# Performance work log

Measured on AMD Instinct MI355X. Metric: run time of the kernel, lower is better.

The kernel has to match this reference:

```python
import jax, jax.numpy as jnp
import numpy as np

L = 2          # num_hidden_layers
B, S, H = 2, 2048, 1024
NH, DH = 16, 64   # heads, head dim
FF = 4096
EPS = 1e-5


def setup_inputs() -> dict:
    key = jax.random.key(0)
    ks = jax.random.split(key, 20)
    s = 0.02
    inp = {
        "hidden_states": jax.random.normal(ks[0], (B, S, H), jnp.float32),
        "attention_mask": jnp.zeros((B, 1, 1, S), jnp.float32),
        "Wq": jax.random.normal(ks[1], (L, H, H), jnp.float32) * s,
        "bq": jnp.zeros((L, H), jnp.float32),
        "Wk": jax.random.normal(ks[2], (L, H, H), jnp.float32) * s,
        "bk": jnp.zeros((L, H), jnp.float32),
        "Wv": jax.random.normal(ks[3], (L, H, H), jnp.float32) * s,
        "bv": jnp.zeros((L, H), jnp.float32),
        "Wao": jax.random.normal(ks[4], (L, H, H), jnp.float32) * s,
        "bao": jnp.zeros((L, H), jnp.float32),
        "ln1_g": jnp.ones((L, H), jnp.float32),
        "ln1_b": jnp.zeros((L, H), jnp.float32),
        "Wi": jax.random.normal(ks[5], (L, H, FF), jnp.float32) * s,
        "bi": jnp.zeros((L, FF), jnp.float32),
        "Wo": jax.random.normal(ks[6], (L, FF, H), jnp.float32) * s,
        "bo": jnp.zeros((L, H), jnp.float32),
        "ln2_g": jnp.ones((L, H), jnp.float32),
        "ln2_b": jnp.zeros((L, H), jnp.float32),
    }
    return inp


def _layernorm(x, g, b):
    m = jnp.mean(x, axis=-1, keepdims=True)
    v = jnp.var(x, axis=-1, keepdims=True)
    return (x - m) * jax.lax.rsqrt(v + EPS) * g + b


def _split_heads(x):
    # [B,S,H] -> [B,NH,S,DH]
    return x.reshape(B, S, NH, DH).transpose(0, 2, 1, 3)


def _layer(x, mask, Wq, bq, Wk, bk, Wv, bv, Wao, bao, g1, b1, Wi, bi, Wo, bo, g2, b2):
    q = _split_heads(x @ Wq + bq)
    k = _split_heads(x @ Wk + bk)
    v = _split_heads(x @ Wv + bv)
    scores = jnp.einsum('bhqd,bhkd->bhqk', q, k) / np.sqrt(DH).astype(np.float32)
    scores = scores + mask  # additive attention mask
    probs = jax.nn.softmax(scores, axis=-1)
    ctx = jnp.einsum('bhqk,bhkd->bhqd', probs, v)
    ctx = ctx.transpose(0, 2, 1, 3).reshape(B, S, H)
    x = _layernorm(ctx @ Wao + bao + x, g1, b1)
    ffn = jax.nn.gelu(x @ Wi + bi, approximate=False) @ Wo + bo
    return _layernorm(ffn + x, g2, b2)


def reference(hidden_states, attention_mask, Wq, bq, Wk, bk, Wv, bv, Wao, bao,
              ln1_g, ln1_b, Wi, bi, Wo, bo, ln2_g, ln2_b):
    x = hidden_states
    for i in range(L):
        x = _layer(x, attention_mask,
                   Wq[i], bq[i], Wk[i], bk[i], Wv[i], bv[i], Wao[i], bao[i],
                   ln1_g[i], ln1_b[i], Wi[i], bi[i], Wo[i], bo[i], ln2_g[i], ln2_b[i])
    return x
```

## Files before the change

### kernel.cpp

```cpp
#include <hip/hip_runtime.h>

typedef _Float16 half_t;
typedef _Float16 half8  __attribute__((ext_vector_type(8)));
typedef _Float16 half4v __attribute__((ext_vector_type(4)));
typedef float    f32x4  __attribute__((ext_vector_type(4)));

#define AS1 __attribute__((address_space(1)))
#define AS3 __attribute__((address_space(3)))

#define MODE_H16  0
#define MODE_F32R 1
#define MODE_GELU 2

__device__ __forceinline__ f32x4 zero4() {
    f32x4 z; z[0] = 0.f; z[1] = 0.f; z[2] = 0.f; z[3] = 0.f; return z;
}

__device__ __forceinline__ half8 lds_frag(const half_t* p) {
    union { uint4 u; half8 h; } c;
    c.u = *(const uint4*)p;
    return c.h;
}

__device__ __forceinline__ void gl_lds16(const half_t* g, half_t* l) {
    __builtin_amdgcn_global_load_lds(
        (AS1 unsigned int*)(unsigned long long)(const void*)g,
        (AS3 unsigned int*)l,
        16, 0, 0);
}

__global__ __launch_bounds__(256) void gemm_bt(
    const half_t* __restrict__ A,
    const half_t* __restrict__ Bt,
    const float*  __restrict__ bias,
    const float*  __restrict__ res,
    void* __restrict__ out,
    int M, int N, int K, int mode)
{
    __shared__ __align__(16) half_t As[128 * 32];
    __shared__ __align__(16) half_t Bs[128 * 32];

    const int tid  = threadIdx.x;
    const int w    = tid >> 6, lane = tid & 63;
    const int m0   = blockIdx.y * 128, n0 = blockIdx.x * 128;
    const int lr   = lane >> 2;
    const int lc   = (lane & 3) * 8;
    const int g    = lane >> 4, ml = lane & 15;
    const int mo   = (w >> 1) * 64, no = (w & 1) * 64;

    f32x4 acc[4][4];
#pragma unroll
    for (int i = 0; i < 4; i++)
#pragma unroll
        for (int j = 0; j < 4; j++) acc[i][j] = zero4();

    const half_t* Ag = A  + (size_t)m0 * K;
    const half_t* Bg = Bt + (size_t)n0 * K;

    for (int k0 = 0; k0 < K; k0 += 32) {
        __syncthreads();
#pragma unroll
        for (int i = 0; i < 2; i++) {
            int r = (w * 2 + i) * 16 + lr;
            gl_lds16(Ag + (size_t)r * K + k0 + lc, &As[(w * 2 + i) * 512]);
            gl_lds16(Bg + (size_t)r * K + k0 + lc, &Bs[(w * 2 + i) * 512]);
        }
        __syncthreads();

        half8 af[4], bf[4];
#pragma unroll
        for (int i = 0; i < 4; i++) af[i] = lds_frag(&As[(mo + i * 16 + ml) * 32 + g * 8]);
#pragma unroll
        for (int j = 0; j < 4; j++) bf[j] = lds_frag(&Bs[(no + j * 16 + ml) * 32 + g * 8]);
#pragma unroll
        for (int i = 0; i < 4; i++)
#pragma unroll
            for (int j = 0; j < 4; j++)
                acc[i][j] = __builtin_amdgcn_mfma_f32_16x16x32_f16(af[i], bf[j], acc[i][j], 0, 0, 0);
    }

    const int gm0 = m0 + mo, gn0 = n0 + no;
#pragma unroll
    for (int j = 0; j < 4; j++) {
        int col = gn0 + j * 16 + ml;
        float bv = bias[col];
#pragma unroll
        for (int i = 0; i < 4; i++) {
#pragma unroll
            for (int r = 0; r < 4; r++) {
                int row = gm0 + i * 16 + g * 4 + r;
                float v = acc[i][j][r] + bv;
                size_t idx = (size_t)row * N + col;
                if (mode == MODE_F32R) {
                    ((float*)out)[idx] = v + res[idx];
                } else if (mode == MODE_GELU) {
                    v = 0.5f * v * (1.f + erff(v * 0.70710678118654752f));
                    ((half_t*)out)[idx] = (half_t)v;
                } else {
                    ((half_t*)out)[idx] = (half_t)v;
                }
            }
        }
    }
}

__global__ __launch_bounds__(256) void gemm_bt64(
    const half_t* __restrict__ A,
    const half_t* __restrict__ Bt,
    const float*  __restrict__ bias,
    const float*  __restrict__ res,
    float* __restrict__ out,
    int M, int N, int K)
{
    __shared__ __align__(16) half_t As[128 * 32];
    __shared__ __align__(16) half_t Bs[64 * 32];

    const int tid  = threadIdx.x;
    const int w    = tid >> 6, lane = tid & 63;
    const int m0   = blockIdx.y * 128, n0 = blockIdx.x * 64;
    const int lr   = lane >> 2, lc = (lane & 3) * 8;
    const int g    = lane >> 4, ml = lane & 15;
    const int mo   = w * 32;

    f32x4 acc[2][4];
#pragma unroll
    for (int i = 0; i < 2; i++)
#pragma unroll
        for (int j = 0; j < 4; j++) acc[i][j] = zero4();

    const half_t* Ag = A  + (size_t)m0 * K;
    const half_t* Bg = Bt + (size_t)n0 * K;

    for (int k0 = 0; k0 < K; k0 += 32) {
        __syncthreads();
#pragma unroll
        for (int i = 0; i < 2; i++)
            gl_lds16(Ag + (size_t)((w * 2 + i) * 16 + lr) * K + k0 + lc, &As[(w * 2 + i) * 512]);
        gl_lds16(Bg + (size_t)(w * 16 + lr) * K + k0 + lc, &Bs[w * 512]);
        __syncthreads();

        half8 af[2], bf[4];
#pragma unroll
        for (int i = 0; i < 2; i++) af[i] = lds_frag(&As[(mo + i * 16 + ml) * 32 + g * 8]);
#pragma unroll
        for (int j = 0; j < 4; j++) bf[j] = lds_frag(&Bs[(j * 16 + ml) * 32 + g * 8]);
#pragma unroll
        for (int i = 0; i < 2; i++)
#pragma unroll
            for (int j = 0; j < 4; j++)
                acc[i][j] = __builtin_amdgcn_mfma_f32_16x16x32_f16(af[i], bf[j], acc[i][j], 0, 0, 0);
    }

    const int gm0 = m0 + mo;
#pragma unroll
    for (int j = 0; j < 4; j++) {
        int col = n0 + j * 16 + ml;
        float bv = bias[col];
#pragma unroll
        for (int i = 0; i < 2; i++) {
#pragma unroll
            for (int r = 0; r < 4; r++) {
                int row = gm0 + i * 16 + g * 4 + r;
                size_t idx = (size_t)row * N + col;
                out[idx] = acc[i][j][r] + bv + res[idx];
            }
        }
    }
}

__global__ __launch_bounds__(256) void gemm_qkv(
    const half_t* __restrict__ A,
    const half_t* __restrict__ Bt,
    const float*  __restrict__ bq,
    const float*  __restrict__ bk,
    const float*  __restrict__ bv,
    half_t* __restrict__ Qo, half_t* __restrict__ Ko, half_t* __restrict__ Vto,
    int M, int K)
{
    __shared__ __align__(16) half_t As[128 * 32];
    __shared__ __align__(16) half_t Bs[128 * 32];

    const int tid  = threadIdx.x;
    const int w    = tid >> 6, lane = tid & 63;
    const int m0   = blockIdx.y * 128, n0 = blockIdx.x * 128;
    const int lr   = lane >> 2, lc = (lane & 3) * 8;
    const int g    = lane >> 4, ml = lane & 15;
    const int mo   = (w >> 1) * 64, no = (w & 1) * 64;

    f32x4 acc[4][4];
#pragma unroll
    for (int i = 0; i < 4; i++)
#pragma unroll
        for (int j = 0; j < 4; j++) acc[i][j] = zero4();

    const half_t* Ag = A  + (size_t)m0 * K;
    const half_t* Bg = Bt + (size_t)n0 * K;

    for (int k0 = 0; k0 < K; k0 += 32) {
        __syncthreads();
#pragma unroll
        for (int i = 0; i < 2; i++) {
            int r = (w * 2 + i) * 16 + lr;
            gl_lds16(Ag + (size_t)r * K + k0 + lc, &As[(w * 2 + i) * 512]);
            gl_lds16(Bg + (size_t)r * K + k0 + lc, &Bs[(w * 2 + i) * 512]);
        }
        __syncthreads();

        half8 af[4], bf[4];
#pragma unroll
        for (int i = 0; i < 4; i++) af[i] = lds_frag(&As[(mo + i * 16 + ml) * 32 + g * 8]);
#pragma unroll
        for (int j = 0; j < 4; j++) bf[j] = lds_frag(&Bs[(no + j * 16 + ml) * 32 + g * 8]);
#pragma unroll
        for (int i = 0; i < 4; i++)
#pragma unroll
            for (int j = 0; j < 4; j++)
                acc[i][j] = __builtin_amdgcn_mfma_f32_16x16x32_f16(af[i], bf[j], acc[i][j], 0, 0, 0);
    }

    const int seg  = n0 >> 10;
    const int nloc = (n0 & 1023) + no;
    const float* bias = (seg == 0) ? bq : (seg == 1) ? bk : bv;
    const int gm0 = m0 + mo;

    if (seg < 2) {
        half_t* O = (seg == 0) ? Qo : Ko;
#pragma unroll
        for (int j = 0; j < 4; j++) {
            int col = nloc + j * 16 + ml;
            float bvv = bias[col];
#pragma unroll
            for (int i = 0; i < 4; i++)
#pragma unroll
                for (int r = 0; r < 4; r++)
                    O[(size_t)(gm0 + i * 16 + g * 4 + r) * 1024 + col] =
                        (half_t)(acc[i][j][r] + bvv);
        }
    } else {
#pragma unroll
        for (int j = 0; j < 4; j++) {
            int col = nloc + j * 16 + ml;
            float bvv = bias[col];
#pragma unroll
            for (int i = 0; i < 4; i++) {
                int rowb = gm0 + i * 16 + g * 4;
                int bb = rowb >> 11, sl = rowb & 2047;
                half4v v;
#pragma unroll
                for (int r = 0; r < 4; r++) v[r] = (half_t)(acc[i][j][r] + bvv);
                *(half4v*)&Vto[((size_t)bb * 1024 + col) * 2048 + sl] = v;
            }
        }
    }
}

__global__ __launch_bounds__(256, 2) void flash_attn(
    const half_t* __restrict__ Q,
    const half_t* __restrict__ Kq,
    const half_t* __restrict__ Vt,
    const float*  __restrict__ mask,
    half_t* __restrict__ ctx,
    int S, int H)
{
    __shared__ __align__(16) half_t Ks[64 * 64];
    __shared__ __align__(16) half_t Vs[64 * 64];
    __shared__ __align__(16) half_t Ps[4 * 32 * 64];

    const int qt = blockIdx.x, h = blockIdx.y, b = blockIdx.z;
    const int tid = threadIdx.x, w = tid >> 6, lane = tid & 63;
    const int g = lane >> 4, ml = lane & 15, m7 = ml & 7;

    const int q0 = qt * 128 + w * 32;
    const half_t* Qg = Q  + ((size_t)(b * S + q0)) * H + h * 64;
    const half_t* Kg = Kq + ((size_t)b * S) * H + h * 64;
    const half_t* Vg = Vt + ((size_t)b * H + h * 64) * (size_t)S;
    const float*  mk = mask + (size_t)b * S;

    half8 qf[2][2];
#pragma unroll
    for (int qi = 0; qi < 2; qi++)
#pragma unroll
        for (int kk = 0; kk < 2; kk++)
            qf[qi][kk] = *(const half8*)(Qg + (size_t)(qi * 16 + ml) * H + kk * 32 + g * 8);

    float m_[2] = {-1e30f, -1e30f}, l_[2] = {0.f, 0.f};
    f32x4 o[2][4];
#pragma unroll
    for (int qi = 0; qi < 2; qi++)
#pragma unroll
        for (int df = 0; df < 4; df++) o[qi][df] = zero4();

    half_t* Pw = &Ps[w * 32 * 64];
    const int srow = tid >> 3;
    const int sc   = tid & 7;

    for (int kv0 = 0; kv0 < S; kv0 += 64) {
        __syncthreads();
#pragma unroll
        for (int t = 0; t < 2; t++) {
            int row = t * 32 + srow;
            int ck  = sc ^ (row & 7);
            gl_lds16(Kg + (size_t)(kv0 + row) * H + ck * 8, &Ks[(t * 256 + w * 64) * 8]);
            gl_lds16(Vg + (size_t)row * S + kv0 + ck * 8,   &Vs[(t * 256 + w * 64) * 8]);
        }
        __syncthreads();

        f32x4 s[2][4];
#pragma unroll
        for (int kvf = 0; kvf < 4; kvf++) {
            half8 k0 = lds_frag(&Ks[(kvf * 16 + ml) * 64 + ((0 + g) ^ m7) * 8]);
            half8 k1 = lds_frag(&Ks[(kvf * 16 + ml) * 64 + ((4 + g) ^ m7) * 8]);
            s[0][kvf] = __builtin_amdgcn_mfma_f32_16x16x32_f16(k0, qf[0][0], zero4(), 0, 0, 0);
            s[0][kvf] = __builtin_amdgcn_mfma_f32_16x16x32_f16(k1, qf[0][1], s[0][kvf], 0, 0, 0);
            s[1][kvf] = __builtin_amdgcn_mfma_f32_16x16x32_f16(k0, qf[1][0], zero4(), 0, 0, 0);
            s[1][kvf] = __builtin_amdgcn_mfma_f32_16x16x32_f16(k1, qf[1][1], s[1][kvf], 0, 0, 0);
        }
#pragma unroll
        for (int kvf = 0; kvf < 4; kvf++) {
            float4 mv = *(const float4*)(mk + kv0 + kvf * 16 + g * 4);
#pragma unroll
            for (int qi = 0; qi < 2; qi++) {
                s[qi][kvf][0] = s[qi][kvf][0] * 0.125f + mv.x;
                s[qi][kvf][1] = s[qi][kvf][1] * 0.125f + mv.y;
                s[qi][kvf][2] = s[qi][kvf][2] * 0.125f + mv.z;
                s[qi][kvf][3] = s[qi][kvf][3] * 0.125f + mv.w;
            }
        }
        float alpha[2];
#pragma unroll
        for (int qi = 0; qi < 2; qi++) {
            float mx = -1e30f;
#pragma unroll
            for (int kvf = 0; kvf < 4; kvf++)
#pragma unroll
                for (int r = 0; r < 4; r++) mx = fmaxf(mx, s[qi][kvf][r]);
            mx = fmaxf(mx, __shfl_xor(mx, 16));
            mx = fmaxf(mx, __shfl_xor(mx, 32));
            float mnew = fmaxf(m_[qi], mx);
            alpha[qi]  = __expf(m_[qi] - mnew);
            m_[qi] = mnew;
            float ps = 0.f;
#pragma unroll
            for (int kvf = 0; kvf < 4; kvf++)
#pragma unroll
                for (int r = 0; r < 4; r++) {
                    float pv = __expf(s[qi][kvf][r] - mnew);
                    s[qi][kvf][r] = pv; ps += pv;
                }
            ps += __shfl_xor(ps, 16);
            ps += __shfl_xor(ps, 32);
            l_[qi] = l_[qi] * alpha[qi] + ps;
#pragma unroll
            for (int kvf = 0; kvf < 4; kvf++) {
                half4v pk;
#pragma unroll
                for (int r = 0; r < 4; r++) pk[r] = (half_t)s[qi][kvf][r];
                *(half4v*)(Pw + (qi * 16 + ml) * 64 +
                           (((kvf * 2 + (g >> 1)) ^ m7) * 8) + (g & 1) * 4) = pk;
            }
        }
#pragma unroll
        for (int qi = 0; qi < 2; qi++) {
#pragma unroll
            for (int r = 0; r < 4; r++) {
                float a = __shfl(alpha[qi], (lane & 48) + g * 4 + r);
#pragma unroll
                for (int df = 0; df < 4; df++) o[qi][df][r] *= a;
            }
        }
#pragma unroll
        for (int kk = 0; kk < 2; kk++) {
            half8 pa0 = lds_frag(&Pw[(ml)      * 64 + ((kk * 4 + g) ^ m7) * 8]);
            half8 pa1 = lds_frag(&Pw[(16 + ml) * 64 + ((kk * 4 + g) ^ m7) * 8]);
#pragma unroll
            for (int df = 0; df < 4; df++) {
                half8 vb = lds_frag(&Vs[(df * 16 + ml) * 64 + ((kk * 4 + g) ^ m7) * 8]);
                o[0][df] = __builtin_amdgcn_mfma_f32_16x16x32_f16(pa0, vb, o[0][df], 0, 0, 0);
                o[1][df] = __builtin_amdgcn_mfma_f32_16x16x32_f16(pa1, vb, o[1][df], 0, 0, 0);
            }
        }
    }

#pragma unroll
    for (int qi = 0; qi < 2; qi++) {
        float inv = 1.f / l_[qi];
#pragma unroll
        for (int r = 0; r < 4; r++) {
            float iv = __shfl(inv, (lane & 48) + g * 4 + r);
            int row = b * S + q0 + qi * 16 + g * 4 + r;
#pragma unroll
            for (int df = 0; df < 4; df++)
                ctx[(size_t)row * H + h * 64 + df * 16 + ml] = (half_t)(o[qi][df][r] * iv);
        }
    }
}

__global__ __launch_bounds__(256) void transpose_cast(
    const float* __restrict__ W, half_t* __restrict__ Wt, int Kd, int Nd)
{
    __shared__ float tile[32][33];
    size_t zoff = (size_t)blockIdx.z * Kd * Nd;
    const float* Wz = W + zoff;
    half_t* Wtz = Wt + zoff;
    int n0 = blockIdx.x * 32, k0 = blockIdx.y * 32;
    int tx = threadIdx.x & 31, ty = threadIdx.x >> 5;
#pragma unroll
    for (int j = 0; j < 4; j++)
        tile[ty + j * 8][tx] = Wz[(size_t)(k0 + ty + j * 8) * Nd + n0 + tx];
    __syncthreads();
#pragma unroll
    for (int j = 0; j < 4; j++)
        Wtz[(size_t)(n0 + ty + j * 8) * Kd + k0 + tx] = (half_t)tile[tx][ty + j * 8];
}

__global__ __launch_bounds__(256) void transpose_qkv(
    const float* __restrict__ Wq, const float* __restrict__ Wk,
    const float* __restrict__ Wv, half_t* __restrict__ WT)
{
    __shared__ float tile[32][33];
    int z = blockIdx.z, l = z / 3, which = z % 3;
    const float* W = ((which == 0) ? Wq : (which == 1) ? Wk : Wv) + (size_t)l * 1024 * 1024;
    half_t* D = WT + ((size_t)l * 3 + which) * 1024 * 1024;
    int n0 = blockIdx.x * 32, k0 = blockIdx.y * 32;
    int tx = threadIdx.x & 31, ty = threadIdx.x >> 5;
#pragma unroll
    for (int j = 0; j < 4; j++)
        tile[ty + j * 8][tx] = W[(size_t)(k0 + ty + j * 8) * 1024 + n0 + tx];
    __syncthreads();
#pragma unroll
    for (int j = 0; j < 4; j++)
        D[(size_t)(n0 + ty + j * 8) * 1024 + k0 + tx] = (half_t)tile[tx][ty + j * 8];
}

__global__ __launch_bounds__(256) void cast_f32_f16(
    const float* __restrict__ in, half_t* __restrict__ out)
{
    int i = blockIdx.x * 256 + threadIdx.x;
    float4 v = ((const float4*)in)[i];
    half4v o; o[0] = (half_t)v.x; o[1] = (half_t)v.y; o[2] = (half_t)v.z; o[3] = (half_t)v.w;
    *(half4v*)(out + (size_t)i * 4) = o;
}

__global__ __launch_bounds__(256) void layernorm_k(
    const float* __restrict__ in,
    const float* __restrict__ gam, const float* __restrict__ bet,
    float* __restrict__ outf, half_t* __restrict__ outh)
{
    int row = blockIdx.x, tid = threadIdx.x;
    const float4 v = ((const float4*)(in + (size_t)row * 1024))[tid];
    float s = v.x + v.y + v.z + v.w;
    float q = v.x * v.x + v.y * v.y + v.z * v.z + v.w * v.w;
    for (int off = 32; off; off >>= 1) { s += __shfl_down(s, off); q += __shfl_down(q, off); }
    __shared__ float ss[4], sq[4];
    int w = tid >> 6;
    if ((tid & 63) == 0) { ss[w] = s; sq[w] = q; }
    __syncthreads();
    float S_ = ss[0] + ss[1] + ss[2] + ss[3];
    float Q_ = sq[0] + sq[1] + sq[2] + sq[3];
    float mean = S_ * (1.f / 1024.f);
    float var  = Q_ * (1.f / 1024.f) - mean * mean;
    float rstd = rsqrtf(var + 1e-5f);
    float4 gm = ((const float4*)gam)[tid];
    float4 bt = ((const float4*)bet)[tid];
    float y0 = (v.x - mean) * rstd * gm.x + bt.x;
    float y1 = (v.y - mean) * rstd * gm.y + bt.y;
    float y2 = (v.z - mean) * rstd * gm.z + bt.z;
    float y3 = (v.w - mean) * rstd * gm.w + bt.w;
    ((float4*)(outf + (size_t)row * 1024))[tid] = make_float4(y0, y1, y2, y3);
    half4v oh; oh[0] = (half_t)y0; oh[1] = (half_t)y1; oh[2] = (half_t)y2; oh[3] = (half_t)y3;
    *(half4v*)(outh + (size_t)row * 1024 + tid * 4) = oh;
}

extern "C" void kernel_launch(void* const* d_in, const int* in_sizes, int n_in,
                              void* d_out, int out_size, void* d_ws, size_t ws_size,
                              hipStream_t stream)
{
    const int Lc = 2, Bb = 2, S = 2048, Hh = 1024, NH = 16, FF = 4096;
    const int M = Bb * S;

    const float* hs   = (const float*)d_in[0];
    const float* mask = (const float*)d_in[1];
    const float* Wq   = (const float*)d_in[2];  const float* bq  = (const float*)d_in[3];
    const float* Wk   = (const float*)d_in[4];  const float* bk  = (const float*)d_in[5];
    const float* Wv   = (const float*)d_in[6];  const float* bv  = (const float*)d_in[7];
    const float* Wao  = (const float*)d_in[8];  const float* bao = (const float*)d_in[9];
    const float* g1   = (const float*)d_in[10]; const float* b1  = (const float*)d_in[11];
    const float* Wi   = (const float*)d_in[12]; const float* bi  = (const float*)d_in[13];
    const float* Wo   = (const float*)d_in[14]; const float* bo  = (const float*)d_in[15];
    const float* g2   = (const float*)d_in[16]; const float* b2  = (const float*)d_in[17];

    char* p = (char*)d_ws;
    auto take = [&](size_t bytes) { char* r = p; p += (bytes + 255) & ~(size_t)255; return r; };

    half_t* WqkvT = (half_t*)take((size_t)Lc * 3 * Hh * Hh * 2);
    half_t* WaoT  = (half_t*)take((size_t)Lc * Hh * Hh * 2);
    half_t* WiT   = (half_t*)take((size_t)Lc * Hh * FF * 2);
    half_t* WoT   = (half_t*)take((size_t)Lc * FF * Hh * 2);
    half_t* xb    = (half_t*)take((size_t)M * Hh * 2);
    half_t* Qb    = (half_t*)take((size_t)M * Hh * 2);
    half_t* Kb2   = (half_t*)take((size_t)M * Hh * 2);
    half_t* Vtb   = (half_t*)take((size_t)M * Hh * 2);
    (void)          take((size_t)M * Hh * 2);
    half_t* h1    = Qb;
    float*  t0    = (float*)take((size_t)M * Hh * 4);
    float*  x1f   = (float*)take((size_t)M * Hh * 4);
    half_t* x1b   = (half_t*)take((size_t)M * Hh * 2);

    dim3 tb(256);

    transpose_qkv<<<dim3(32, 32, Lc * 3), tb, 0, stream>>>(Wq, Wk, Wv, WqkvT);
    transpose_cast<<<dim3(32, 32, Lc), tb, 0, stream>>>(Wao, WaoT, Hh, Hh);
    transpose_cast<<<dim3(FF / 32, 32, Lc), tb, 0, stream>>>(Wi, WiT, Hh, FF);
    transpose_cast<<<dim3(32, FF / 32, Lc), tb, 0, stream>>>(Wo, WoT, FF, Hh);
    cast_f32_f16<<<dim3(M * Hh / 1024), tb, 0, stream>>>(hs, xb);

    const float* xres = hs;
    for (int l = 0; l < Lc; l++) {
        const half_t* WqkvTl = WqkvT + (size_t)l * 3 * Hh * Hh;
        const half_t* WaoTl  = WaoT  + (size_t)l * Hh * Hh;
        const half_t* WiTl   = WiT   + (size_t)l * Hh * FF;
        const half_t* WoTl   = WoT   + (size_t)l * FF * Hh;

        gemm_qkv<<<dim3(3072 / 128, M / 128), tb, 0, stream>>>(
            xb, WqkvTl, bq + l * Hh, bk + l * Hh, bv + l * Hh, Qb, Kb2, Vtb, M, Hh);

        flash_attn<<<dim3(S / 128, NH, Bb), tb, 0, stream>>>(Qb, Kb2, Vtb, mask, xb, S, Hh);

        gemm_bt64<<<dim3(Hh / 64, M / 128), tb, 0, stream>>>(
            xb, WaoTl, bao + l * Hh, xres, t0, M, Hh, Hh);
        layernorm_k<<<dim3(M), tb, 0, stream>>>(t0, g1 + l * Hh, b1 + l * Hh, x1f, x1b);

        gemm_bt<<<dim3(FF / 128, M / 128), tb, 0, stream>>>(
            x1b, WiTl, bi + l * FF, nullptr, h1, M, FF, Hh, MODE_GELU);
        gemm_bt64<<<dim3(Hh / 64, M / 128), tb, 0, stream>>>(
            h1, WoTl, bo + l * Hh, x1f, t0, M, Hh, FF);

        float* outf = (l == Lc - 1) ? (float*)d_out : x1f;
        layernorm_k<<<dim3(M), tb, 0, stream>>>(t0, g2 + l * Hh, b2 + l * Hh, outf, xb);
        xres = x1f;
    }
}
```

Measured before the change: 830.2 us.

## Double GEMM K-tile to 64 with XOR-swizzled LDS and tanh-form GELU

All three GEMM kernels now stage 64-wide K slices instead of 32, which halves the number of barrier pairs per output tile. The LDS layout uses an XOR swizzle on 16-byte chunks so that fragment reads avoid bank conflicts. The exact erf GELU is replaced by a sigmoid-form tanh approximation built on __expf. The costs are doubled LDS use, which may reduce occupancy, and a small numerical deviation from exact GELU.

```diff
diff --git a/kernel.cpp b/kernel.cpp
--- a/kernel.cpp
+++ b/kernel.cpp
@@ -20,6 +20,12 @@
     union { uint4 u; half8 h; } c;
     c.u = *(const uint4*)p;
     return c.h;
+}
+
+__device__ __forceinline__ float gelu_f(float v) {
+    float t = v * v;
+    float u = v * (1.595769122f + 0.0713548163f * t);
+    return v / (1.f + __expf(-u));
 }
 
 __device__ __forceinline__ void gl_lds16(const half_t* g, half_t* l) {
@@ -28,6 +34,7 @@
         (AS3 unsigned int*)l,
         16, 0, 0);
 }
+
 
 __global__ __launch_bounds__(256) void gemm_bt(
     const half_t* __restrict__ A,
@@ -37,16 +44,16 @@
     void* __restrict__ out,
     int M, int N, int K, int mode)
 {
-    __shared__ __align__(16) half_t As[128 * 32];
-    __shared__ __align__(16) half_t Bs[128 * 32];
+    __shared__ __align__(16) half_t As[128 * 64];
+    __shared__ __align__(16) half_t Bs[128 * 64];
 
     const int tid  = threadIdx.x;
     const int w    = tid >> 6, lane = tid & 63;
     const int m0   = blockIdx.y * 128, n0 = blockIdx.x * 128;
-    const int lr   = lane >> 2;
-    const int lc   = (lane & 3) * 8;
-    const int g    = lane >> 4, ml = lane & 15;
+    const int g    = lane >> 4, ml = lane & 15, m7 = ml & 7;
     const int mo   = (w >> 1) * 64, no = (w & 1) * 64;
+    const int r8   = lane >> 3;
+    const int sck  = ((lane & 7) ^ (r8 & 7)) * 8;
 
     f32x4 acc[4][4];
 #pragma unroll
@@ -57,26 +64,29 @@
     const half_t* Ag = A  + (size_t)m0 * K;
     const half_t* Bg = Bt + (size_t)n0 * K;
 
-    for (int k0 = 0; k0 < K; k0 += 32) {
-        __syncthreads();
-#pragma unroll
-        for (int i = 0; i < 2; i++) {
-            int r = (w * 2 + i) * 16 + lr;
-            gl_lds16(Ag + (size_t)r * K + k0 + lc, &As[(w * 2 + i) * 512]);
-            gl_lds16(Bg + (size_t)r * K + k0 + lc, &Bs[(w * 2 + i) * 512]);
-        }
-        __syncthreads();
-
-        half8 af[4], bf[4];
-#pragma unroll
-        for (int i = 0; i < 4; i++) af[i] = lds_frag(&As[(mo + i * 16 + ml) * 32 + g * 8]);
-#pragma unroll
-        for (int j = 0; j < 4; j++) bf[j] = lds_frag(&Bs[(no + j * 16 + ml) * 32 + g * 8]);
-#pragma unroll
-        for (int i = 0; i < 4; i++)
-#pragma unroll
-            for (int j = 0; j < 4; j++)
-                acc[i][j] = __builtin_amdgcn_mfma_f32_16x16x32_f16(af[i], bf[j], acc[i][j], 0, 0, 0);
+    for (int k0 = 0; k0 < K; k0 += 64) {
+        __syncthreads();
+#pragma unroll
+        for (int i = 0; i < 4; i++) {
+            int t = w * 4 + i;
+            gl_lds16(Ag + (size_t)(t * 8 + r8) * K + k0 + sck, &As[t * 512]);
+            gl_lds16(Bg + (size_t)(t * 8 + r8) * K + k0 + sck, &Bs[t * 512]);
+        }
+        __syncthreads();
+#pragma unroll
+        for (int kk = 0; kk < 2; kk++) {
+            const int co = ((kk * 4 + g) ^ m7) * 8;
+            half8 af[4], bf[4];
+#pragma unroll
+            for (int i = 0; i < 4; i++) af[i] = lds_frag(&As[(mo + i * 16 + ml) * 64 + co]);
+#pragma unroll
+            for (int j = 0; j < 4; j++) bf[j] = lds_frag(&Bs[(no + j * 16 + ml) * 64 + co]);
+#pragma unroll
+            for (int i = 0; i < 4; i++)
+#pragma unroll
+                for (int j = 0; j < 4; j++)
+                    acc[i][j] = __builtin_amdgcn_mfma_f32_16x16x32_f16(af[i], bf[j], acc[i][j], 0, 0, 0);
+        }
     }
 
     const int gm0 = m0 + mo, gn0 = n0 + no;
@@ -94,8 +104,7 @@
                 if (mode == MODE_F32R) {
                     ((float*)out)[idx] = v + res[idx];
                 } else if (mode == MODE_GELU) {
-                    v = 0.5f * v * (1.f + erff(v * 0.70710678118654752f));
-                    ((half_t*)out)[idx] = (half_t)v;
+                    ((half_t*)out)[idx] = (half_t)gelu_f(v);
                 } else {
                     ((half_t*)out)[idx] = (half_t)v;
                 }
@@ -112,15 +121,16 @@
     float* __restrict__ out,
     int M, int N, int K)
 {
-    __shared__ __align__(16) half_t As[128 * 32];
-    __shared__ __align__(16) half_t Bs[64 * 32];
+    __shared__ __align__(16) half_t As[128 * 64];
+    __shared__ __align__(16) half_t Bs[64 * 64];
 
     const int tid  = threadIdx.x;
     const int w    = tid >> 6, lane = tid & 63;
     const int m0   = blockIdx.y * 128, n0 = blockIdx.x * 64;
-    const int lr   = lane >> 2, lc = (lane & 3) * 8;
-    const int g    = lane >> 4, ml = lane & 15;
+    const int g    = lane >> 4, ml = lane & 15, m7 = ml & 7;
     const int mo   = w * 32;
+    const int r8   = lane >> 3;
+    const int sck  = ((lane & 7) ^ (r8 & 7)) * 8;
 
     f32x4 acc[2][4];
 #pragma unroll
@@ -131,24 +141,33 @@
     const half_t* Ag = A  + (size_t)m0 * K;
     const half_t* Bg = Bt + (size_t)n0 * K;
 
-    for (int k0 = 0; k0 < K; k0 += 32) {
-        __syncthreads();
-#pragma unroll
-        for (int i = 0; i < 2; i++)
-            gl_lds16(Ag + (size_t)((w * 2 + i) * 16 + lr) * K + k0 + lc, &As[(w * 2 + i) * 512]);
-        gl_lds16(Bg + (size_t)(w * 16 + lr) * K + k0 + lc, &Bs[w * 512]);
-        __syncthreads();
-
-        half8 af[2], bf[4];
-#pragma unroll
-        for (int i = 0; i < 2; i++) af[i] = lds_frag(&As[(mo + i * 16 + ml) * 32 + g * 8]);
-#pragma unroll
-        for (int j = 0; j < 4; j++) bf[j] = lds_frag(&Bs[(j * 16 + ml) * 32 + g * 8]);
-#pragma unroll
-        for (int i = 0; i < 2; i++)
-#pragma unroll
-            for (int j = 0; j < 4; j++)
-                acc[i][j] = __builtin_amdgcn_mfma_f32_16x16x32_f16(af[i], bf[j], acc[i][j], 0, 0, 0);
+    for (int k0 = 0; k0 < K; k0 += 64) {
+        __syncthreads();
+#pragma unroll
+        for (int i = 0; i < 4; i++) {
+            int t = w * 4 + i;
+            gl_lds16(Ag + (size_t)(t * 8 + r8) * K + k0 + sck, &As[t * 512]);
+        }
+#pragma unroll
+        for (int i = 0; i < 2; i++) {
+            int t = w * 2 + i;
+            gl_lds16(Bg + (size_t)(t * 8 + r8) * K + k0 + sck, &Bs[t * 512]);
+        }
+        __syncthreads();
+#pragma unroll
+        for (int kk = 0; kk < 2; kk++) {
+            const int co = ((kk * 4 + g) ^ m7) * 8;
+            half8 af[2], bf[4];
+#pragma unroll
+            for (int i = 0; i < 2; i++) af[i] = lds_frag(&As[(mo + i * 16 + ml) * 64 + co]);
+#pragma unroll
+            for (int j = 0; j < 4; j++) bf[j] = lds_frag(&Bs[(j * 16 + ml) * 64 + co]);
+#pragma unroll
+            for (int i = 0; i < 2; i++)
+#pragma unroll
+                for (int j = 0; j < 4; j++)
+                    acc[i][j] = __builtin_amdgcn_mfma_f32_16x16x32_f16(af[i], bf[j], acc[i][j], 0, 0, 0);
+        }
     }
 
     const int gm0 = m0 + mo;
@@ -177,15 +196,16 @@
     half_t* __restrict__ Qo, half_t* __restrict__ Ko, half_t* __restrict__ Vto,
     int M, int K)
 {
-    __shared__ __align__(16) half_t As[128 * 32];
-    __shared__ __align__(16) half_t Bs[128 * 32];
+    __shared__ __align__(16) half_t As[128 * 64];
+    __shared__ __align__(16) half_t Bs[128 * 64];
 
     const int tid  = threadIdx.x;
     const int w    = tid >> 6, lane = tid & 63;
     const int m0   = blockIdx.y * 128, n0 = blockIdx.x * 128;
-    const int lr   = lane >> 2, lc = (lane & 3) * 8;
-    const int g    = lane >> 4, ml = lane & 15;
+    const int g    = lane >> 4, ml = lane & 15, m7 = ml & 7;
     const int mo   = (w >> 1) * 64, no = (w & 1) * 64;
+    const int r8   = lane >> 3;
+    const int sck  = ((lane & 7) ^ (r8 & 7)) * 8;
 
     f32x4 acc[4][4];
 #pragma unroll
@@ -196,26 +216,29 @@
     const half_t* Ag = A  + (size_t)m0 * K;
     const half_t* Bg = Bt + (size_t)n0 * K;
 
-    for (int k0 = 0; k0 < K; k0 += 32) {
-        __syncthreads();
-#pragma unroll
-        for (int i = 0; i < 2; i++) {
-            int r = (w * 2 + i) * 16 + lr;
-            gl_lds16(Ag + (size_t)r * K + k0 + lc, &As[(w * 2 + i) * 512]);
-            gl_lds16(Bg + (size_t)r * K + k0 + lc, &Bs[(w * 2 + i) * 512]);
-        }
-        __syncthreads();
-
-        half8 af[4], bf[4];
-#pragma unroll
-        for (int i = 0; i < 4; i++) af[i] = lds_frag(&As[(mo + i * 16 + ml) * 32 + g * 8]);
-#pragma unroll
-        for (int j = 0; j < 4; j++) bf[j] = lds_frag(&Bs[(no + j * 16 + ml) * 32 + g * 8]);
-#pragma unroll
-        for (int i = 0; i < 4; i++)
-#pragma unroll
-            for (int j = 0; j < 4; j++)
-                acc[i][j] = __builtin_amdgcn_mfma_f32_16x16x32_f16(af[i], bf[j], acc[i][j], 0, 0, 0);
+    for (int k0 = 0; k0 < K; k0 += 64) {
+        __syncthreads();
+#pragma unroll
+        for (int i = 0; i < 4; i++) {
+            int t = w * 4 + i;
+            gl_lds16(Ag + (size_t)(t * 8 + r8) * K + k0 + sck, &As[t * 512]);
+            gl_lds16(Bg + (size_t)(t * 8 + r8) * K + k0 + sck, &Bs[t * 512]);
+        }
+        __syncthreads();
+#pragma unroll
+        for (int kk = 0; kk < 2; kk++) {
+            const int co = ((kk * 4 + g) ^ m7) * 8;
+            half8 af[4], bf[4];
+#pragma unroll
+            for (int i = 0; i < 4; i++) af[i] = lds_frag(&As[(mo + i * 16 + ml) * 64 + co]);
+#pragma unroll
+            for (int j = 0; j < 4; j++) bf[j] = lds_frag(&Bs[(no + j * 16 + ml) * 64 + co]);
+#pragma unroll
+            for (int i = 0; i < 4; i++)
+#pragma unroll
+                for (int j = 0; j < 4; j++)
+                    acc[i][j] = __builtin_amdgcn_mfma_f32_16x16x32_f16(af[i], bf[j], acc[i][j], 0, 0, 0);
+        }
     }
 
     const int seg  = n0 >> 10;
```

Result: faster. 749.5 us (-9.7%).
